# Kernel tuning notes

Measured on AMD Instinct MI355X. Metric: run time of the kernel, lower is better.

The kernel has to match this reference:

```python
import jax, jax.numpy as jnp
import numpy as np

BATCH = 4096
IN_DIMS = (128, 128)   # input spatial dims (H, W)
W_DIMS = (16, 16)      # weight_dims from init_kwargs


def setup_inputs() -> dict:
    key = jax.random.key(0)
    k1, k2 = jax.random.split(key)
    inputs = jax.random.normal(k1, (BATCH,) + IN_DIMS, dtype=jnp.float32)
    w = jax.random.normal(k2, W_DIMS, dtype=jnp.float32)
    return {"inputs": inputs, "w": w}


def reference(inputs, w):
    # GTPCA_Layer.call_input_larger with project=True (shift transform,
    # input dims strictly larger than weight dims).
    B, H, W = inputs.shape
    kh, kw = w.shape
    n = jnp.asarray(H * W, dtype=inputs.dtype)  # self.n = prod(input_dims)

    # weights = w / sqrt(sum(w^2) / n)
    wn = w / jnp.sqrt(jnp.sum(w * w) / n)

    # scores = valid cross-correlation(inputs, wn) / n  -> (B, H-kh+1, W-kw+1)
    scores = jax.lax.conv_general_dilated(
        inputs[:, None, :, :], wn[None, None, :, :],
        window_strides=(1, 1), padding='VALID',
        dimension_numbers=('NCHW', 'OIHW', 'NCHW'))[:, 0] / n
    sh, sw = scores.shape[1], scores.shape[2]

    # first-occurrence argmax of |scores| over spatial dims (matches the
    # cumsum <= 1 trick in get_argmax: jnp.argmax returns first max)
    flat_abs = jnp.abs(scores).reshape(B, -1)
    idx = jnp.argmax(flat_abs, axis=-1)          # (B,)
    rows = idx // sw
    cols = idx % sw

    # gather_nd(scores, argmax, batch_dims=1)
    smax = jnp.take_along_axis(scores.reshape(B, -1), idx[:, None], axis=-1)[:, 0]

    # per-sample dynamic pad of wn to input_dims with offset = argmax
    # (tf.map_fn(tf.pad(weights, [argmax, max_argmax-argmax-1])))
    def pad_one(r, c):
        return jax.lax.dynamic_update_slice(
            jnp.zeros((H, W), dtype=inputs.dtype), wn, (r, c))

    wpad = jax.vmap(pad_one)(rows, cols)         # (B, H, W)

    # output = score_at_argmax * padded weights
    return smax[:, None, None] * wpad
```

## Files before the change

kernel.cpp:

```cpp
#include <hip/hip_runtime.h>
#include <math.h>

#define H 128
#define SW 113
#define CAND_CAP 128

typedef __attribute__((ext_vector_type(8))) short short8;
typedef __attribute__((ext_vector_type(4))) float f32x4;

static __device__ __forceinline__ uint32_t f2bf1(float v) {
    uint32_t u = __float_as_uint(v);
    return (u + 0x7fffu + ((u >> 16) & 1u)) >> 16;
}
static __device__ __forceinline__ uint32_t pack2(float a, float b) {
    return f2bf1(a) | (f2bf1(b) << 16);
}
static __device__ __forceinline__ float bf2f_lo(uint32_t d) {
    return __uint_as_float(d << 16);
}
static __device__ __forceinline__ float bf2f_hi(uint32_t d) {
    return __uint_as_float(d & 0xffff0000u);
}

__global__ __launch_bounds__(256) void prep_wn(const float* __restrict__ w,
                                               float* __restrict__ wn) {
    __shared__ float red[256];
    int t = threadIdx.x;
    float wv = w[t];
    red[t] = wv * wv;
    __syncthreads();
    for (int off = 128; off > 0; off >>= 1) {
        if (t < off) red[t] += red[t + off];
        __syncthreads();
    }
    float denom = sqrtf(red[0] / 16384.0f);
    wn[t] = wv / denom;
}

__global__ __launch_bounds__(256) void gtpca_main(
    const float* __restrict__ in, const float* __restrict__ wn_g,
    float* __restrict__ out) {

    __shared__ __align__(16) uint32_t lds[8192];
    float* red_a  = (float*)lds;
    int*   cand_n = (int*)(lds + 256);
    int*   cand_i = (int*)(lds + 260);
    float* cand_v = (float*)(lds + 260 + CAND_CAP);

    const int tid  = threadIdx.x;
    const int lane = tid & 63;
    const int wid  = tid >> 6;
    const int b    = blockIdx.x;
    const float* ip  = in + (size_t)b * (H * H);
    const float4* in4 = (const float4*)ip;

    const int n15 = lane & 15;
    const int kg  = lane >> 4;

#pragma unroll
    for (int i = 0; i < 16; ++i) {
        int g = tid + 256 * i;
        float4 v = in4[g];
        int r = g >> 5, h = g & 31;
        int phys = (h >> 1) ^ (r & 15);
        uint2 pk2 = make_uint2(pack2(v.x, v.y), pack2(v.z, v.w));
        *(uint2*)(lds + r * 64 + phys * 4 + (h & 1) * 2) = pk2;
    }

    short8 Breg[16];
#pragma unroll
    for (int ki = 0; ki < 16; ++ki) {
        short8 f;
#pragma unroll
        for (int e = 0; e < 8; ++e) {
            int d = kg * 8 + e - n15;
            float v = ((unsigned)d < 16u) ? wn_g[ki * 16 + d] : 0.0f;
            f[e] = (short)f2bf1(v);
        }
        Breg[ki] = f;
    }
    __syncthreads();

    const short8* ldsA = (const short8*)lds;
    uint32_t pk[32];
    float best_a = -1.0f;
#pragma unroll
    for (int tyi = 0; tyi < 2; ++tyi) {
        int ty = 2 * wid + tyi;
        int rbase = 16 * ty + n15;
#pragma unroll
        for (int hf = 0; hf < 2; ++hf) {
            f32x4 C[4];
            f32x4 Cz = {0.0f, 0.0f, 0.0f, 0.0f};
#pragma unroll
            for (int j = 0; j < 4; ++j) C[j] = Cz;
#pragma unroll
            for (int ki = 0; ki < 16; ++ki) {
                int r = rbase + ki; if (r > 127) r = 127;
                int rx = r << 4, rk = r & 15;
#pragma unroll
                for (int j = 0; j < 4; ++j) {
                    int cl = 2 * (4 * hf + j) + kg;
                    if (cl > 15) cl = 15;
                    short8 a = ldsA[rx | (cl ^ rk)];
                    C[j] = __builtin_amdgcn_mfma_f32_16x16x32_bf16(a, Breg[ki], C[j], 0, 0, 0);
                }
            }
            int ybase = 16 * ty + 4 * kg;
#pragma unroll
            for (int j = 0; j < 4; ++j) {
                int x = 16 * (4 * hf + j) + n15;
                if (x < SW) {
#pragma unroll
                    for (int ri = 0; ri < 4; ++ri) {
                        int y = ybase + ri;
                        if (y < SW) {
                            float a = fabsf(C[j][ri]);
                            if (a > best_a) best_a = a;
                        }
                    }
                }
                pk[((tyi * 2 + hf) * 4 + j) * 2 + 0] = pack2(C[j][0], C[j][1]);
                pk[((tyi * 2 + hf) * 4 + j) * 2 + 1] = pack2(C[j][2], C[j][3]);
            }
        }
    }
    __syncthreads();

    red_a[tid] = best_a;
    if (tid == 0) *cand_n = 0;
    __syncthreads();
    for (int off = 128; off > 0; off >>= 1) {
        if (tid < off) red_a[tid] = fmaxf(red_a[tid], red_a[tid + off]);
        __syncthreads();
    }
    const float tau = red_a[0] - 48.0f;

#pragma unroll
    for (int tyi = 0; tyi < 2; ++tyi) {
#pragma unroll
        for (int hf = 0; hf < 2; ++hf) {
#pragma unroll
            for (int j = 0; j < 4; ++j) {
                int x = 16 * (4 * hf + j) + n15;
                if (x < SW) {
                    int ybase = 16 * (2 * wid + tyi) + 4 * kg;
#pragma unroll
                    for (int p = 0; p < 2; ++p) {
                        uint32_t d = pk[((tyi * 2 + hf) * 4 + j) * 2 + p];
                        float v0 = bf2f_lo(d);
                        float v1 = bf2f_hi(d);
                        int y0 = ybase + 2 * p;
                        if (y0 < SW && fabsf(v0) >= tau) {
                            int pos = atomicAdd(cand_n, 1);
                            if (pos < CAND_CAP) cand_i[pos] = y0 * SW + x;
                        }
                        if (y0 + 1 < SW && fabsf(v1) >= tau) {
                            int pos = atomicAdd(cand_n, 1);
                            if (pos < CAND_CAP) cand_i[pos] = (y0 + 1) * SW + x;
                        }
                    }
                }
            }
        }
    }
    __syncthreads();
    int ncand = *cand_n; if (ncand > CAND_CAP) ncand = CAND_CAP;

    for (int c = wid; c < ncand; c += 4) {
        int idx = cand_i[c];
        int yy = idx / SW, xx = idx - yy * SW;
        int kj = lane & 15, k0 = (lane >> 4) * 4;
        float s = 0.0f;
#pragma unroll
        for (int j2 = 0; j2 < 4; ++j2) {
            int ki = k0 + j2;
            s = __builtin_fmaf(ip[(yy + ki) * H + xx + kj], wn_g[ki * 16 + kj], s);
        }
#pragma unroll
        for (int mk = 32; mk > 0; mk >>= 1) s += __shfl_xor(s, mk, 64);
        if (lane == 0) cand_v[c] = s;
    }
    __syncthreads();

    float bsa = -1.0f, bsv = 0.0f; int bsi = 0x7FFFFFFF;
    for (int c = 0; c < ncand; ++c) {
        float v = cand_v[c], a = fabsf(v);
        int idx = cand_i[c];
        if (a > bsa || (a == bsa && idx < bsi)) { bsa = a; bsi = idx; bsv = v; }
    }
    const int rr = bsi / SW;
    const int cc = bsi - rr * SW;
    const float sv = bsv * (1.0f / 16384.0f);

    float4* out4 = (float4*)(out + (size_t)b * (H * H));
#pragma unroll
    for (int i = 0; i < 16; ++i) {
        int g = tid + i * 256;
        int orow = g >> 5;
        int ocol = (g & 31) << 2;
        float4 v = {0.0f, 0.0f, 0.0f, 0.0f};
        int dr = orow - rr;
        if ((unsigned)dr < 16u) {
            float* vp = (float*)&v;
#pragma unroll
            for (int k = 0; k < 4; ++k) {
                int dc = ocol + k - cc;
                if ((unsigned)dc < 16u) vp[k] = sv * wn_g[dr * 16 + dc];
            }
        }
        out4[g] = v;
    }
}

extern "C" void kernel_launch(void* const* d_in, const int* in_sizes, int n_in,
                              void* d_out, int out_size, void* d_ws, size_t ws_size,
                              hipStream_t stream) {
    const float* in = (const float*)d_in[0];
    const float* w = (const float*)d_in[1];
    float* out = (float*)d_out;
    float* wn = (float*)d_ws;

    prep_wn<<<1, 256, 0, stream>>>(w, wn);
    gtpca_main<<<4096, 256, 0, stream>>>(in, wn, out);
}
```

Baseline: 500.8 us.

## Precompute MFMA weight fragments and streamline argmax threshold reduction

Moves per-block construction of the bf16 weight MFMA fragments into the prep kernel, storing them in a global array that each block loads directly. It replaces software bf16 rounding with the hardware packed convert instruction and precomputes LDS swizzle offsets. The |score| max is now taken on packed bf16 integers with wave shuffles and a 4-entry LDS reduce instead of an 8-step barrier tree. Invalid border positions are masked once, and threads whose local max is below the threshold skip the candidate scan. This adds a global fragment table dependency and relies on the masking exactly matching the valid region.

```diff
diff --git a/kernel.cpp b/kernel.cpp
--- a/kernel.cpp
+++ b/kernel.cpp
@@ -8,12 +8,16 @@
 typedef __attribute__((ext_vector_type(8))) short short8;
 typedef __attribute__((ext_vector_type(4))) float f32x4;
 
+__device__ short8 Breg_g[16][64];
+
 static __device__ __forceinline__ uint32_t f2bf1(float v) {
     uint32_t u = __float_as_uint(v);
     return (u + 0x7fffu + ((u >> 16) & 1u)) >> 16;
 }
-static __device__ __forceinline__ uint32_t pack2(float a, float b) {
-    return f2bf1(a) | (f2bf1(b) << 16);
+static __device__ __forceinline__ uint32_t cvtpk(float lo, float hi) {
+    uint32_t r;
+    asm("v_cvt_pk_bf16_f32 %0, %1, %2" : "=v"(r) : "v"(lo), "v"(hi));
+    return r;
 }
 static __device__ __forceinline__ float bf2f_lo(uint32_t d) {
     return __uint_as_float(d << 16);
@@ -33,8 +37,21 @@
         if (t < off) red[t] += red[t + off];
         __syncthreads();
     }
-    float denom = sqrtf(red[0] / 16384.0f);
-    wn[t] = wv / denom;
+    float inv = 1.0f / sqrtf(red[0] / 16384.0f);
+    wn[t] = wv * inv;
+    for (int q = 0; q < 4; ++q) {
+        int pair = t * 4 + q;
+        int ki = pair >> 6, ln = pair & 63;
+        int nn = ln & 15, kgq = ln >> 4;
+        short8 f;
+#pragma unroll
+        for (int e = 0; e < 8; ++e) {
+            int d = kgq * 8 + e - nn;
+            float v = ((unsigned)d < 16u) ? w[ki * 16 + d] * inv : 0.0f;
+            f[e] = (short)f2bf1(v);
+        }
+        Breg_g[ki][ln] = f;
+    }
 }
 
 __global__ __launch_bounds__(256) void gtpca_main(
@@ -42,10 +59,10 @@
     float* __restrict__ out) {
 
     __shared__ __align__(16) uint32_t lds[8192];
-    float* red_a  = (float*)lds;
-    int*   cand_n = (int*)(lds + 256);
-    int*   cand_i = (int*)(lds + 260);
-    float* cand_v = (float*)(lds + 260 + CAND_CAP);
+    uint32_t* redu  = lds;
+    int*   cand_n = (int*)(lds + 8);
+    int*   cand_i = (int*)(lds + 16);
+    float* cand_v = (float*)(lds + 16 + CAND_CAP);
 
     const int tid  = threadIdx.x;
     const int lane = tid & 63;
@@ -63,27 +80,24 @@
         float4 v = in4[g];
         int r = g >> 5, h = g & 31;
         int phys = (h >> 1) ^ (r & 15);
-        uint2 pk2 = make_uint2(pack2(v.x, v.y), pack2(v.z, v.w));
+        uint2 pk2 = make_uint2(cvtpk(v.x, v.y), cvtpk(v.z, v.w));
         *(uint2*)(lds + r * 64 + phys * 4 + (h & 1) * 2) = pk2;
     }
 
     short8 Breg[16];
 #pragma unroll
-    for (int ki = 0; ki < 16; ++ki) {
-        short8 f;
-#pragma unroll
-        for (int e = 0; e < 8; ++e) {
-            int d = kg * 8 + e - n15;
-            float v = ((unsigned)d < 16u) ? wn_g[ki * 16 + d] : 0.0f;
-            f[e] = (short)f2bf1(v);
-        }
-        Breg[ki] = f;
-    }
-    __syncthreads();
-
-    const short8* ldsA = (const short8*)lds;
+    for (int ki = 0; ki < 16; ++ki) Breg[ki] = Breg_g[ki][lane];
+
+    int xoff[8];
+#pragma unroll
+    for (int T = 0; T < 8; ++T) {
+        int cl = 2 * T + kg; if (cl > 15) cl = 15;
+        xoff[T] = cl << 4;
+    }
+    __syncthreads();
+
+    const char* ldsc = (const char*)lds;
     uint32_t pk[32];
-    float best_a = -1.0f;
 #pragma unroll
     for (int tyi = 0; tyi < 2; ++tyi) {
         int ty = 2 * wid + tyi;
@@ -97,53 +111,61 @@
 #pragma unroll
             for (int ki = 0; ki < 16; ++ki) {
                 int r = rbase + ki; if (r > 127) r = 127;
-                int rx = r << 4, rk = r & 15;
+                int base = (r << 8) ^ ((r & 15) << 4);
 #pragma unroll
                 for (int j = 0; j < 4; ++j) {
-                    int cl = 2 * (4 * hf + j) + kg;
-                    if (cl > 15) cl = 15;
-                    short8 a = ldsA[rx | (cl ^ rk)];
+                    short8 a = *(const short8*)(ldsc + (base ^ xoff[4 * hf + j]));
                     C[j] = __builtin_amdgcn_mfma_f32_16x16x32_bf16(a, Breg[ki], C[j], 0, 0, 0);
                 }
             }
-            int ybase = 16 * ty + 4 * kg;
 #pragma unroll
             for (int j = 0; j < 4; ++j) {
-                int x = 16 * (4 * hf + j) + n15;
-                if (x < SW) {
-#pragma unroll
-                    for (int ri = 0; ri < 4; ++ri) {
-                        int y = ybase + ri;
-                        if (y < SW) {
-                            float a = fabsf(C[j][ri]);
-                            if (a > best_a) best_a = a;
-                        }
-                    }
-                }
-                pk[((tyi * 2 + hf) * 4 + j) * 2 + 0] = pack2(C[j][0], C[j][1]);
-                pk[((tyi * 2 + hf) * 4 + j) * 2 + 1] = pack2(C[j][2], C[j][3]);
-            }
-        }
-    }
-    __syncthreads();
-
-    red_a[tid] = best_a;
+                pk[((tyi * 2 + hf) * 4 + j) * 2 + 0] = cvtpk(C[j][0], C[j][1]);
+                pk[((tyi * 2 + hf) * 4 + j) * 2 + 1] = cvtpk(C[j][2], C[j][3]);
+            }
+        }
+    }
+
+    if (n15 != 0) { pk[14] = 0; pk[15] = 0; pk[30] = 0; pk[31] = 0; }
+    if (wid == 3) {
+        uint32_t keep = (kg == 0) ? 0x0000ffffu : 0u;
+#pragma unroll
+        for (int q = 16; q < 32; q += 2) { pk[q] &= keep; pk[q + 1] = 0; }
+    }
+
+    uint32_t mself = 0;
+#pragma unroll
+    for (int q = 0; q < 32; ++q) {
+        uint32_t a = pk[q] & 0x7fff7fffu;
+        uint32_t h2 = a >> 16, l2 = a & 0xffffu;
+        mself = mself > h2 ? mself : h2;
+        mself = mself > l2 ? mself : l2;
+    }
+    uint32_t mw = mself;
+#pragma unroll
+    for (int mk = 32; mk; mk >>= 1) {
+        uint32_t o = (uint32_t)__shfl_xor((int)mw, mk, 64);
+        if (o > mw) mw = o;
+    }
+
+    __syncthreads();
+    if (lane == 0) redu[wid] = mw;
     if (tid == 0) *cand_n = 0;
     __syncthreads();
-    for (int off = 128; off > 0; off >>= 1) {
-        if (tid < off) red_a[tid] = fmaxf(red_a[tid], red_a[tid + off]);
-        __syncthreads();
-    }
-    const float tau = red_a[0] - 48.0f;
-
-#pragma unroll
-    for (int tyi = 0; tyi < 2; ++tyi) {
-#pragma unroll
-        for (int hf = 0; hf < 2; ++hf) {
-#pragma unroll
-            for (int j = 0; j < 4; ++j) {
-                int x = 16 * (4 * hf + j) + n15;
-                if (x < SW) {
+    uint32_t mall = redu[0];
+    { uint32_t t1 = redu[1]; if (t1 > mall) mall = t1;
+      t1 = redu[2]; if (t1 > mall) mall = t1;
+      t1 = redu[3]; if (t1 > mall) mall = t1; }
+    const float tau = __uint_as_float(mall << 16) - 48.0f;
+
+    if (__uint_as_float(mself << 16) >= tau) {
+#pragma unroll
+        for (int tyi = 0; tyi < 2; ++tyi) {
+#pragma unroll
+            for (int hf = 0; hf < 2; ++hf) {
+#pragma unroll
+                for (int j = 0; j < 4; ++j) {
+                    int x = 16 * (4 * hf + j) + n15;
                     int ybase = 16 * (2 * wid + tyi) + 4 * kg;
 #pragma unroll
                     for (int p = 0; p < 2; ++p) {
@@ -151,11 +173,11 @@
                         float v0 = bf2f_lo(d);
                         float v1 = bf2f_hi(d);
                         int y0 = ybase + 2 * p;
-                        if (y0 < SW && fabsf(v0) >= tau) {
+                        if (fabsf(v0) >= tau) {
                             int pos = atomicAdd(cand_n, 1);
                             if (pos < CAND_CAP) cand_i[pos] = y0 * SW + x;
                         }
-                        if (y0 + 1 < SW && fabsf(v1) >= tau) {
+                        if (fabsf(v1) >= tau) {
                             int pos = atomicAdd(cand_n, 1);
                             if (pos < CAND_CAP) cand_i[pos] = (y0 + 1) * SW + x;
                         }
```

After: 473.2 us. 1.06x faster.
